# Kernel optimization log

Measured on AMD Instinct MI355X. Metric: run time of the kernel, lower is better.

Reference implementation:

```python
import jax, jax.numpy as jnp
import numpy as np

B, N, H, D = 16, 512, 8, 128  # batch, nodes, heads, hid_dim (per-head dim == hid_dim)


def setup_inputs() -> dict:
    key = jax.random.key(0)
    ks = jax.random.split(key, 12)
    x = jax.random.normal(ks[0], (B, N, D), dtype=jnp.float32)
    dist = jax.random.normal(ks[1], (B, N, N), dtype=jnp.float32)
    mask = (jax.random.uniform(ks[2], (B, N)) < 0.9).astype(jnp.float32)
    w_std = 0.02
    Wq = jax.random.normal(ks[3], (D, H * D), dtype=jnp.float32) * w_std
    Wk = jax.random.normal(ks[4], (D, H * D), dtype=jnp.float32) * w_std
    Wv = jax.random.normal(ks[5], (D, H * D), dtype=jnp.float32) * w_std
    Wo = jax.random.normal(ks[6], (H * D, D), dtype=jnp.float32) * w_std
    bq = jax.random.normal(ks[7], (H * D,), dtype=jnp.float32) * w_std
    bk = jax.random.normal(ks[8], (H * D,), dtype=jnp.float32) * w_std
    bv = jax.random.normal(ks[9], (H * D,), dtype=jnp.float32) * w_std
    bo = jax.random.normal(ks[10], (D,), dtype=jnp.float32) * w_std
    return {"x": x, "dist": dist, "mask": mask,
            "Wq": Wq, "bq": bq, "Wk": Wk, "bk": bk,
            "Wv": Wv, "bv": bv, "Wo": Wo, "bo": bo}


def reference(x, dist, mask, Wq, bq, Wk, bk, Wv, bv, Wo, bo):
    scale = jnp.asarray(D, x.dtype) ** -0.5
    # projections: [B,N,H*D] -> [B,H,N,D]
    q = (x @ Wq + bq).reshape(B, N, H, D).transpose(0, 2, 1, 3)
    k = (x @ Wk + bk).reshape(B, N, H, D).transpose(0, 2, 1, 3)
    v = (x @ Wv + bv).reshape(B, N, H, D).transpose(0, 2, 1, 3)
    m = mask[:, None, :, None]  # [B,1,N,1]
    q = q * m * scale
    k = k * m
    v = v * m
    a = jnp.einsum('bhnd,bhmd->bhnm', q, k)  # [B,H,N,N]
    a = a + dist[:, None, :, :]  # dist bias broadcast over heads
    amask = (mask[:, :, None] * mask[:, None, :])[:, None, :, :]  # [B,1,N,N]
    a = jnp.where(amask == 0, jnp.asarray(-1e9, a.dtype), a)
    a = jax.nn.softmax(a, axis=-1)
    a = jnp.where(amask == 0, jnp.asarray(0.0, a.dtype), a)
    y = jnp.einsum('bhnm,bhmd->bhnd', a, v)
    y = y.transpose(0, 2, 1, 3).reshape(B, N, H * D)
    y = y @ Wo + bo
    return y * mask[:, :, None]
```

## Files before the change

kernel.cpp:

```cpp
#include <hip/hip_runtime.h>
#include <hip/hip_bf16.h>

#define B_ 16
#define N_ 512
#define H_ 8
#define D_ 128
#define HD_ 1024
#define SCALE_ 0.08838834764831845f

typedef __attribute__((ext_vector_type(8))) short bf16x8;
typedef __attribute__((ext_vector_type(4))) float f32x4;
typedef __attribute__((ext_vector_type(4))) _Float16 f16x4;

__device__ __forceinline__ unsigned short f2bf(float f) {
    union { __hip_bfloat16 h; unsigned short u; } cv;
    cv.h = __float2bfloat16(f);
    return cv.u;
}
__device__ __forceinline__ unsigned short f2h(float f) {
    union { _Float16 h; unsigned short u; } cv;
    cv.h = (_Float16)f;
    return cv.u;
}

__global__ __launch_bounds__(256) void prep_kernel(
    const float* __restrict__ Wq, const float* __restrict__ Wk,
    const float* __restrict__ Wv, const float* __restrict__ Wo,
    unsigned short* __restrict__ wTh, unsigned short* __restrict__ woT)
{
    __shared__ float T[32][33];
    const int tile = blockIdx.x;
    const int t = threadIdx.x;
    if (tile < 384) {
        const int w = tile / 128;
        const int rem = tile % 128;
        const int kt = rem & 3;
        const int ct = rem >> 2;
        const float* W = (w == 0) ? Wq : (w == 1) ? Wk : Wv;
        const int k0 = kt * 32, c0 = ct * 32;
        #pragma unroll
        for (int u = 0; u < 4; u++) {
            int lin = t + 256 * u; int r = lin >> 5, c = lin & 31;
            T[r][c] = W[(size_t)(k0 + r) * 1024 + c0 + c];
        }
        __syncthreads();
        unsigned short* oh = wTh + (size_t)w * 131072;
        #pragma unroll
        for (int u = 0; u < 4; u++) {
            int lin = t + 256 * u; int c = lin >> 5, r = lin & 31;
            oh[(size_t)(c0 + c) * 128 + k0 + r] = f2bf(T[r][c]);
        }
    } else {
        const int rem = tile - 384;
        const int nt = rem & 3;
        const int kt = rem >> 2;
        const int k0 = kt * 32, n0 = nt * 32;
        #pragma unroll
        for (int u = 0; u < 4; u++) {
            int lin = t + 256 * u; int r = lin >> 5, c = lin & 31;
            T[r][c] = Wo[(size_t)(k0 + r) * 128 + n0 + c];
        }
        __syncthreads();
        #pragma unroll
        for (int u = 0; u < 4; u++) {
            int lin = t + 256 * u; int c = lin >> 5, r = lin & 31;
            woT[(size_t)(n0 + c) * 1024 + k0 + r] = f2bf(T[r][c]);
        }
    }
}

__global__ __launch_bounds__(256, 2) void qkv_kernel(
    const float* __restrict__ x, const float* __restrict__ mask,
    const unsigned short* __restrict__ wTh,
    const float* __restrict__ bq, const float* __restrict__ bk,
    const float* __restrict__ bv,
    unsigned short* __restrict__ q, unsigned short* __restrict__ k,
    unsigned short* __restrict__ vT)
{
    const int cb = blockIdx.x % 24;
    const int by = blockIdx.x / 24;
    const int row0 = by * 128, c0 = cb * 128;
    const int which = c0 >> 10, w0 = c0 & 1023;
    const float* bi = (which == 0) ? bq : (which == 1) ? bk : bv;

    __shared__ alignas(16) unsigned short Wh[128][136];
    __shared__ float biS[128];
    __shared__ float mskS[128];

    const int t = threadIdx.x;
    if (t < 128) { biS[t] = bi[w0 + t]; mskS[t] = mask[row0 + t]; }

    const unsigned short* whp = wTh + (size_t)which * 131072 + (size_t)w0 * 128;
    #pragma unroll
    for (int u = 0; u < 8; u++) {
        int lin = t + 256 * u; int c = lin >> 4, k8 = (lin & 15) * 8;
        *(bf16x8*)&Wh[c][k8] = *(const bf16x8*)&whp[(size_t)c * 128 + k8];
    }

    const int wave = t >> 6, lane = t & 63, m16 = lane & 15, g4 = lane >> 4;
    const int rw = row0 + wave * 32;

    bf16x8 ah[2][4];
    #pragma unroll
    for (int mt = 0; mt < 2; mt++)
        #pragma unroll
        for (int kc = 0; kc < 4; kc++) {
            const float* xp = &x[(size_t)(rw + mt * 16 + m16) * 128 + kc * 32 + g4 * 8];
            float4 v0 = *(const float4*)xp;
            float4 v1 = *(const float4*)(xp + 4);
            float vv[8] = {v0.x, v0.y, v0.z, v0.w, v1.x, v1.y, v1.z, v1.w};
            union { bf16x8 v; unsigned short s[8]; } Hh;
            #pragma unroll
            for (int e = 0; e < 8; e++) Hh.s[e] = f2bf(vv[e]);
            ah[mt][kc] = Hh.v;
        }
    __syncthreads();

    const f32x4 zero = {0.f, 0.f, 0.f, 0.f};
    f32x4 acc[2][8];
    #pragma unroll
    for (int mt = 0; mt < 2; mt++)
        #pragma unroll
        for (int nt = 0; nt < 8; nt++) acc[mt][nt] = zero;

    #pragma unroll
    for (int nt = 0; nt < 8; nt++) {
        #pragma unroll
        for (int kc = 0; kc < 4; kc++) {
            bf16x8 bh = *(const bf16x8*)&Wh[nt * 16 + m16][kc * 32 + g4 * 8];
            #pragma unroll
            for (int mt = 0; mt < 2; mt++)
                acc[mt][nt] = __builtin_amdgcn_mfma_f32_16x16x32_bf16(ah[mt][kc], bh, acc[mt][nt], 0, 0, 0);
        }
    }
    __syncthreads();

    const int b = row0 >> 9, h = w0 >> 7;
    const int iseq0 = row0 & 511;
    unsigned short* Tr = &Wh[0][0];

    if (which == 2) {
        #pragma unroll
        for (int mt = 0; mt < 2; mt++)
            #pragma unroll
            for (int nt = 0; nt < 8; nt++)
                #pragma unroll
                for (int r = 0; r < 4; r++) {
                    int rowl = wave * 32 + mt * 16 + g4 * 4 + r;
                    int col = nt * 16 + m16;
                    Tr[col * 136 + rowl] = f2h((acc[mt][nt][r] + biS[col]) * mskS[rowl]);
                }
        __syncthreads();
        unsigned short* vbase = vT + (size_t)(b * 8 + h) * 128 * 512 + iseq0;
        #pragma unroll
        for (int u = 0; u < 8; u++) {
            int lin = t + 256 * u; int dl = lin >> 4, i8 = (lin & 15) * 8;
            *(bf16x8*)&vbase[(size_t)dl * 512 + i8] = *(const bf16x8*)&Tr[dl * 136 + i8];
        }
    } else {
        const float sc = (which == 0) ? SCALE_ : 1.0f;
        #pragma unroll
        for (int mt = 0; mt < 2; mt++)
            #pragma unroll
            for (int nt = 0; nt < 8; nt++)
                #pragma unroll
                for (int r = 0; r < 4; r++) {
                    int rowl = wave * 32 + mt * 16 + g4 * 4 + r;
                    int col = nt * 16 + m16;
                    Tr[rowl * 136 + col] = f2bf((acc[mt][nt][r] + biS[col]) * (mskS[rowl] * sc));
                }
        __syncthreads();
        unsigned short* dst = ((which == 0) ? q : k) +
                              ((size_t)(b * 8 + h) * 512 + iseq0) * 128;
        #pragma unroll
        for (int u = 0; u < 8; u++) {
            int lin = t + 256 * u; int rl = lin >> 4, c8 = (lin & 15) * 8;
            *(bf16x8*)&dst[(size_t)rl * 128 + c8] = *(const bf16x8*)&Tr[rl * 136 + c8];
        }
    }
}

__global__ __launch_bounds__(256, 2) void attn_kernel(
    const unsigned short* __restrict__ q, const unsigned short* __restrict__ k,
    const unsigned short* __restrict__ vT, const float* __restrict__ dist,
    const float* __restrict__ mask, unsigned short* __restrict__ y)
{
    const int xid = blockIdx.x;
    const int bh = (xid & 7) | ((xid >> 6) << 3);
    const int itile = (xid >> 3) & 7;
    const int b = bh >> 3, h = bh & 7;
    const int i0 = itile * 64;

    const unsigned short* qb = q + (size_t)bh * 512 * 128;
    const unsigned short* kb = k + (size_t)bh * 512 * 128;
    const unsigned short* vb = vT + (size_t)bh * 128 * 512;

    __shared__ alignas(16) unsigned short Ks[64][136];
    __shared__ alignas(16) unsigned short Vs[128][76];
    __shared__ alignas(16) float cmS[512];

    const int t = threadIdx.x;
    const int wave = t >> 6, lane = t & 63;
    const int m16 = lane & 15, g4 = lane >> 4;
    const int iw = i0 + wave * 16;

    cmS[t] = (mask[b * 512 + t] == 0.0f) ? -1e9f : 0.0f;
    cmS[256 + t] = (mask[b * 512 + 256 + t] == 0.0f) ? -1e9f : 0.0f;

    bf16x8 aq[4];
    #pragma unroll
    for (int c = 0; c < 4; c++)
        aq[c] = *(const bf16x8*)(qb + (size_t)(iw + m16) * 128 + c * 32 + g4 * 8);

    const int krow = t >> 2, kcol = (t & 3) * 32;
    const int vrow = t >> 1, vcol = (t & 1) * 32;

    const float* dbase = dist + ((size_t)b * 512 + iw) * 512;

    float4 dvA[4];
    {
        bf16x8 kp[4], vp[4];
        #pragma unroll
        for (int u = 0; u < 4; u++) {
            kp[u] = *(const bf16x8*)(kb + (size_t)krow * 128 + kcol + u * 8);
            vp[u] = *(const bf16x8*)(vb + (size_t)vrow * 512 + vcol + u * 8);
        }
        #pragma unroll
        for (int jt = 0; jt < 4; jt++)
            dvA[jt] = *(const float4*)&dbase[(size_t)m16 * 512 + jt * 16 + g4 * 4];
        #pragma unroll
        for (int u = 0; u < 4; u++) {
            *(bf16x8*)&Ks[krow][kcol + u * 8] = kp[u];
            union { bf16x8 v8; ushort4 h4[2]; } cv; cv.v8 = vp[u];
            *(ushort4*)&Vs[vrow][vcol + u * 8] = cv.h4[0];
            *(ushort4*)&Vs[vrow][vcol + u * 8 + 4] = cv.h4[1];
        }
    }
    __syncthreads();

    const f32x4 zero = {0.f, 0.f, 0.f, 0.f};
    float rm = -3.0e38f, rl = 0.f;
    f32x4 Ot[8] = {zero, zero, zero, zero, zero, zero, zero, zero};

    for (int c = 0; c < 8; c++) {
        const int j0 = c * 64;
        bf16x8 kp[4], vp[4];
        float4 dvB[4];
        if (c < 7) {
            const int j0n = j0 + 64;
            #pragma unroll
            for (int u = 0; u < 4; u++) {
                kp[u] = *(const bf16x8*)(kb + (size_t)(j0n + krow) * 128 + kcol + u * 8);
                vp[u] = *(const bf16x8*)(vb + (size_t)vrow * 512 + j0n + vcol + u * 8);
            }
            #pragma unroll
            for (int jt = 0; jt < 4; jt++)
                dvB[jt] = *(const float4*)&dbase[(size_t)m16 * 512 + j0n + jt * 16 + g4 * 4];
        }

        f32x4 s[4];
        #pragma unroll
        for (int jt = 0; jt < 4; jt++) {
            float4 cm4 = *(const float4*)&cmS[j0 + jt * 16 + g4 * 4];
            f32x4 a = {dvA[jt].x + cm4.x, dvA[jt].y + cm4.y,
                       dvA[jt].z + cm4.z, dvA[jt].w + cm4.w};
            #pragma unroll
            for (int cc = 0; cc < 4; cc++) {
                bf16x8 kf = *(const bf16x8*)&Ks[jt * 16 + m16][cc * 32 + g4 * 8];
                a = __builtin_amdgcn_mfma_f32_16x16x32_bf16(kf, aq[cc], a, 0, 0, 0);
            }
            s[jt] = a;
        }

        float cm = -3.0e38f;
        #pragma unroll
        for (int jt = 0; jt < 4; jt++)
            #pragma unroll
            for (int r = 0; r < 4; r++) cm = fmaxf(cm, s[jt][r]);
        cm = fmaxf(cm, __shfl_xor(cm, 16));
        cm = fmaxf(cm, __shfl_xor(cm, 32));

        float nm = fmaxf(rm, cm);
        float alpha = __expf(rm - nm);
        rm = nm;
        rl *= alpha;

        f16x4 pa[4];
        float ps = 0.f;
        #pragma unroll
        for (int jt = 0; jt < 4; jt++) {
            #pragma unroll
            for (int r = 0; r < 4; r++) {
                float p = __expf(s[jt][r] - rm);
                ps += p;
                pa[jt][r] = (_Float16)p;
            }
        }
        ps += __shfl_xor(ps, 16);
        ps += __shfl_xor(ps, 32);
        rl += ps;

        float a4[4];
        #pragma unroll
        for (int r = 0; r < 4; r++) a4[r] = __shfl(alpha, g4 * 4 + r);
        #pragma unroll
        for (int dt = 0; dt < 8; dt++)
            #pragma unroll
            for (int r = 0; r < 4; r++) Ot[dt][r] *= a4[r];

        #pragma unroll
        for (int jt = 0; jt < 4; jt++)
            #pragma unroll
            for (int dt = 0; dt < 8; dt++) {
                f16x4 vf = *(const f16x4*)&Vs[dt * 16 + m16][jt * 16 + g4 * 4];
                Ot[dt] = __builtin_amdgcn_mfma_f32_16x16x16f16(pa[jt], vf, Ot[dt], 0, 0, 0);
            }

        if (c < 7) {
            __syncthreads();
            #pragma unroll
            for (int u = 0; u < 4; u++) {
                *(bf16x8*)&Ks[krow][kcol + u * 8] = kp[u];
                union { bf16x8 v8; ushort4 h4[2]; } cv; cv.v8 = vp[u];
                *(ushort4*)&Vs[vrow][vcol + u * 8] = cv.h4[0];
                *(ushort4*)&Vs[vrow][vcol + u * 8 + 4] = cv.h4[1];
            }
            #pragma unroll
            for (int jt = 0; jt < 4; jt++) dvA[jt] = dvB[jt];
            __syncthreads();
        }
    }

    __syncthreads();
    float rs = (rl > 0.f) ? 1.0f / rl : 0.f;
    float rs4[4];
    #pragma unroll
    for (int r = 0; r < 4; r++) rs4[r] = __shfl(rs, g4 * 4 + r);
    #pragma unroll
    for (int dt = 0; dt < 8; dt++)
        #pragma unroll
        for (int r = 0; r < 4; r++)
            Ks[wave * 16 + g4 * 4 + r][dt * 16 + m16] = f2bf(Ot[dt][r] * rs4[r]);
    #pragma unroll
    for (int u = 0; u < 4; u++) {
        int lin = lane + 64 * u;
        int row = lin >> 4, seg = lin & 15;
        *(bf16x8*)&y[((size_t)(b * 512) + iw + row) * 1024 + h * 128 + seg * 8] =
            *(const bf16x8*)&Ks[wave * 16 + row][seg * 8];
    }
}

__global__ __launch_bounds__(256) void oproj_kernel(
    const unsigned short* __restrict__ Y, const unsigned short* __restrict__ woT,
    const float* __restrict__ bo, const float* __restrict__ mask,
    float* __restrict__ out)
{
    const int row0 = blockIdx.x * 32;
    __shared__ alignas(16) unsigned short Ys[32][136];
    __shared__ alignas(16) unsigned short Ws[128][136];
    __shared__ float boS[128];
    __shared__ float mskS[32];

    const int t = threadIdx.x;
    if (t < 128) boS[t] = bo[t];
    if (t < 32) mskS[t] = mask[row0 + t];

    const int wave = t >> 6, lane = t & 63;
    const int m16 = lane & 15, g4 = lane >> 4;
    const int mrow = (wave & 1) * 16, n0 = (wave >> 1) * 64;

    const int yr = t >> 4, yk = (t & 15) * 8;
    const int wn = t >> 4, wk = (t & 15) * 8;

    const f32x4 zero = {0.f, 0.f, 0.f, 0.f};
    f32x4 acc[4] = {zero, zero, zero, zero};

    bf16x8 yp[2], wp[8];
    #pragma unroll
    for (int u = 0; u < 2; u++)
        yp[u] = *(const bf16x8*)&Y[(size_t)(row0 + yr + u * 16) * 1024 + yk];
    #pragma unroll
    for (int u = 0; u < 8; u++)
        wp[u] = *(const bf16x8*)&woT[(size_t)(wn + u * 16) * 1024 + wk];

    for (int c = 0; c < 8; c++) {
        __syncthreads();
        #pragma unroll
        for (int u = 0; u < 2; u++) *(bf16x8*)&Ys[yr + u * 16][yk] = yp[u];
        #pragma unroll
        for (int u = 0; u < 8; u++) *(bf16x8*)&Ws[wn + u * 16][wk] = wp[u];
        __syncthreads();
        if (c < 7) {
            const int kc0 = (c + 1) * 128;
            #pragma unroll
            for (int u = 0; u < 2; u++)
                yp[u] = *(const bf16x8*)&Y[(size_t)(row0 + yr + u * 16) * 1024 + kc0 + yk];
            #pragma unroll
            for (int u = 0; u < 8; u++)
                wp[u] = *(const bf16x8*)&woT[(size_t)(wn + u * 16) * 1024 + kc0 + wk];
        }
        #pragma unroll
        for (int kc = 0; kc < 4; kc++) {
            bf16x8 a = *(const bf16x8*)&Ys[mrow + m16][kc * 32 + g4 * 8];
            #pragma unroll
            for (int nt = 0; nt < 4; nt++) {
                bf16x8 bb = *(const bf16x8*)&Ws[n0 + nt * 16 + m16][kc * 32 + g4 * 8];
                acc[nt] = __builtin_amdgcn_mfma_f32_16x16x32_bf16(a, bb, acc[nt], 0, 0, 0);
            }
        }
    }
    __syncthreads();

    float* Ot = (float*)&Ws[0][0];
    #pragma unroll
    for (int nt = 0; nt < 4; nt++)
        #pragma unroll
        for (int r = 0; r < 4; r++) {
            int rowl = mrow + g4 * 4 + r;
            int col = n0 + nt * 16 + m16;
            Ot[rowl * 132 + col] = (acc[nt][r] + boS[col]) * mskS[rowl];
        }
    __syncthreads();
    #pragma unroll
    for (int u = 0; u < 4; u++) {
        int lin = t + 256 * u; int r = lin >> 5, c4 = lin & 31;
        *(float4*)&out[(size_t)(row0 + r) * 128 + c4 * 4] =
            *(const float4*)&Ot[r * 132 + c4 * 4];
    }
}

extern "C" void kernel_launch(void* const* d_in, const int* in_sizes, int n_in,
                              void* d_out, int out_size, void* d_ws, size_t ws_size,
                              hipStream_t stream) {
    const float* x    = (const float*)d_in[0];
    const float* dist = (const float*)d_in[1];
    const float* mask = (const float*)d_in[2];
    const float* Wq   = (const float*)d_in[3];
    const float* bq   = (const float*)d_in[4];
    const float* Wk   = (const float*)d_in[5];
    const float* bk   = (const float*)d_in[6];
    const float* Wv   = (const float*)d_in[7];
    const float* bv   = (const float*)d_in[8];
    const float* Wo   = (const float*)d_in[9];
    const float* bo   = (const float*)d_in[10];
    float* out = (float*)d_out;

    const size_t per = (size_t)B_ * H_ * N_ * D_;
    unsigned short* qb  = (unsigned short*)d_ws;
    unsigned short* kb  = qb + per;
    unsigned short* vb  = kb + per;
    unsigned short* yb  = vb + per;
    unsigned short* wTh = yb + per;
    unsigned short* woT = wTh + 3 * 131072;

    prep_kernel<<<512, 256, 0, stream>>>(Wq, Wk, Wv, Wo, wTh, woT);
    qkv_kernel<<<1536, 256, 0, stream>>>(x, mask, wTh, bq, bk, bv, qb, kb, vb);
    attn_kernel<<<1024, 256, 0, stream>>>(qb, kb, vb, dist, mask, yb);
    oproj_kernel<<<256, 256, 0, stream>>>(yb, woT, bo, mask, out);
}
```

Before: 159.5 us.

## Stage P through LDS and use 16x16x32 f16 MFMA for PV product

Softmax probabilities are written to a per-wave LDS buffer so they can be reloaded in the layout the wider 16x16x32 f16 MFMA needs. This halves the number of PV MFMA instructions and uses 8-wide V reads from LDS. V rows are repadded to 72 so V can be stored with single 16-byte writes. The price is an extra LDS write and read of P per tile, and the P exchange within a wave depends on lockstep execution with no explicit barrier.

```diff
diff --git a/kernel.cpp b/kernel.cpp
--- a/kernel.cpp
+++ b/kernel.cpp
@@ -10,7 +10,7 @@
 
 typedef __attribute__((ext_vector_type(8))) short bf16x8;
 typedef __attribute__((ext_vector_type(4))) float f32x4;
-typedef __attribute__((ext_vector_type(4))) _Float16 f16x4;
+typedef __attribute__((ext_vector_type(8))) _Float16 f16x8;
 
 __device__ __forceinline__ unsigned short f2bf(float f) {
     union { __hip_bfloat16 h; unsigned short u; } cv;
@@ -196,7 +196,8 @@
     const unsigned short* vb = vT + (size_t)bh * 128 * 512;
 
     __shared__ alignas(16) unsigned short Ks[64][136];
-    __shared__ alignas(16) unsigned short Vs[128][76];
+    __shared__ alignas(16) unsigned short Vs[128][72];
+    __shared__ alignas(16) unsigned short Ps[4][16][72];
     __shared__ alignas(16) float cmS[512];
 
     const int t = threadIdx.x;
@@ -231,9 +232,7 @@
         #pragma unroll
         for (int u = 0; u < 4; u++) {
             *(bf16x8*)&Ks[krow][kcol + u * 8] = kp[u];
-            union { bf16x8 v8; ushort4 h4[2]; } cv; cv.v8 = vp[u];
-            *(ushort4*)&Vs[vrow][vcol + u * 8] = cv.h4[0];
-            *(ushort4*)&Vs[vrow][vcol + u * 8 + 4] = cv.h4[1];
+            *(bf16x8*)&Vs[vrow][vcol + u * 8] = vp[u];
         }
     }
     __syncthreads();
@@ -285,16 +284,17 @@
         rm = nm;
         rl *= alpha;
 
-        f16x4 pa[4];
         float ps = 0.f;
         #pragma unroll
         for (int jt = 0; jt < 4; jt++) {
-            #pragma unroll
-            for (int r = 0; r < 4; r++) {
-                float p = __expf(s[jt][r] - rm);
-                ps += p;
-                pa[jt][r] = (_Float16)p;
-            }
+            float p0 = __expf(s[jt][0] - rm);
+            float p1 = __expf(s[jt][1] - rm);
+            float p2 = __expf(s[jt][2] - rm);
+            float p3 = __expf(s[jt][3] - rm);
+            ps += (p0 + p1) + (p2 + p3);
+            ushort4 w;
+            w.x = f2h(p0); w.y = f2h(p1); w.z = f2h(p2); w.w = f2h(p3);
+            *(ushort4*)&Ps[wave][m16][(jt * 4 + g4) * 4] = w;
         }
         ps += __shfl_xor(ps, 16);
         ps += __shfl_xor(ps, 32);
@@ -309,21 +309,21 @@
             for (int r = 0; r < 4; r++) Ot[dt][r] *= a4[r];
 
         #pragma unroll
-        for (int jt = 0; jt < 4; jt++)
+        for (int c32 = 0; c32 < 2; c32++) {
+            f16x8 af = *(const f16x8*)&Ps[wave][m16][c32 * 32 + g4 * 8];
             #pragma unroll
             for (int dt = 0; dt < 8; dt++) {
-                f16x4 vf = *(const f16x4*)&Vs[dt * 16 + m16][jt * 16 + g4 * 4];
-                Ot[dt] = __builtin_amdgcn_mfma_f32_16x16x16f16(pa[jt], vf, Ot[dt], 0, 0, 0);
+                f16x8 vf = *(const f16x8*)&Vs[dt * 16 + m16][c32 * 32 + g4 * 8];
+                Ot[dt] = __builtin_amdgcn_mfma_f32_16x16x32_f16(af, vf, Ot[dt], 0, 0, 0);
             }
+        }
 
         if (c < 7) {
             __syncthreads();
             #pragma unroll
             for (int u = 0; u < 4; u++) {
                 *(bf16x8*)&Ks[krow][kcol + u * 8] = kp[u];
-                union { bf16x8 v8; ushort4 h4[2]; } cv; cv.v8 = vp[u];
-                *(ushort4*)&Vs[vrow][vcol + u * 8] = cv.h4[0];
-                *(ushort4*)&Vs[vrow][vcol + u * 8 + 4] = cv.h4[1];
+                *(bf16x8*)&Vs[vrow][vcol + u * 8] = vp[u];
             }
             #pragma unroll
             for (int jt = 0; jt < 4; jt++) dvA[jt] = dvB[jt];
```

New measurement: 163.5 us. +2.5%, slower.
